# Performance work log

Measured on AMD Instinct MI355X. Metric: run time of the kernel, lower is better.

The kernel has to match this reference:

```python
import jax, jax.numpy as jnp
import numpy as np

N, D, H, C, E, M = 8192, 256, 256, 64, 262144, 2048
WD = 5e-4   # weight_decay
HP1 = 0.9
TAU = 0.5


def _l2norm(x, eps=1e-12):
    n = jnp.sqrt(jnp.sum(x * x, axis=1, keepdims=True))
    return x / jnp.maximum(n, eps)


def setup_inputs() -> dict:
    key = jax.random.key(0)
    ks = jax.random.split(key, 20)
    s = 0.05
    return dict(
        features=jax.random.uniform(ks[0], (N, D), dtype=jnp.float32),
        support=jax.random.uniform(ks[1], (N, N), dtype=jnp.float32) / N,  # mimics normalized adjacency scale
        labels=jax.random.uniform(ks[2], (N, C), dtype=jnp.float32),
        mat01_intra=jax.random.uniform(ks[3], (M, M), dtype=jnp.float32),
        mat01_inter=jax.random.uniform(ks[4], (M, M), dtype=jnp.float32),
        W0=jax.random.normal(ks[5], (D, H), dtype=jnp.float32) * s,
        b0=jnp.zeros((H,), jnp.float32),
        W1=jax.random.normal(ks[6], (H, C), dtype=jnp.float32) * s,
        b1=jnp.zeros((C,), jnp.float32),
        Wh0=jax.random.normal(ks[7], (D, H), dtype=jnp.float32) * s,
        bh0=jnp.zeros((H,), jnp.float32),
        Wh1=jax.random.normal(ks[8], (H, C), dtype=jnp.float32) * s,
        bh1=jnp.zeros((C,), jnp.float32),
        Wc=jax.random.normal(ks[9], (2 * C, 1), dtype=jnp.float32) * s,
        bc=jnp.zeros((1,), jnp.float32),
        edge_pos_i=jax.random.randint(ks[10], (E,), 0, N, dtype=jnp.int32),
        edge_pos_j=jax.random.randint(ks[11], (E,), 0, N, dtype=jnp.int32),
        train_idx=jax.random.randint(ks[12], (M,), 0, N, dtype=jnp.int32),
        mask=jax.random.randint(ks[13], (N,), 0, 2, dtype=jnp.int32),
    )


def _forward(features, support, labels, mat01_intra, mat01_inter,
             W0, b0, W1, b1, Wh0, bh0, Wh1, bh1, Wc, bc,
             edge_pos_i, edge_pos_j, train_idx, mask):
    # --- GCN branch: relu(S (X W0) + b0) -> S (h0 W1) + b1
    h0 = jax.nn.relu(support @ (features @ W0) + b0)
    h1 = support @ (h0 @ W1) + b1
    gcn_n = _l2norm(h1)
    # --- HGCN branch (2-layer GCN stand-in)
    g0 = jax.nn.relu(support @ (features @ Wh0) + bh0)
    hgcn = support @ (g0 @ Wh1) + bh1
    hgcn_n = _l2norm(hgcn)
    outputs = _l2norm(0.6 * gcn_n + 0.4 * hgcn_n)

    # masked softmax cross entropy
    maskf = mask.astype(jnp.float32)
    maskf = maskf / jnp.mean(maskf)
    logp = jax.nn.log_softmax(outputs, axis=1)
    loss_ce = jnp.mean(-jnp.sum(labels * logp, axis=1) * maskf)

    # edge gathers + contra MLP: log sigmoid of linear on concatenated pairs
    yi_g, yj_g = gcn_n[edge_pos_i], gcn_n[edge_pos_j]
    yi_h, yj_h = hgcn_n[edge_pos_i], hgcn_n[edge_pos_j]
    z1 = jnp.concatenate([yi_g, yj_h], axis=1) @ Wc + bc  # [E,1]
    z2 = jnp.concatenate([yi_h, yj_g], axis=1) @ Wc + bc
    p_e_xy = -jnp.mean(jax.nn.log_sigmoid(z1)) - jnp.mean(jax.nn.log_sigmoid(z2))

    # unsupervised contrastive over full NxN
    cd1 = jnp.exp((gcn_n @ hgcn_n.T) / TAU)      # [N,N]
    pn1 = jnp.diagonal(cd1) / jnp.mean(cd1, axis=1)
    cd2 = jnp.exp((hgcn_n @ gcn_n.T) / TAU)
    pn2 = jnp.diagonal(cd2) / jnp.mean(cd2, axis=1)
    contra = -HP1 * jnp.mean(jnp.log(jnp.concatenate([pn1, pn2], axis=0)))

    # supervised contrastive on train subset
    rowsum = jnp.sum(mat01_intra, axis=1)  # mat01_intra_rowsum buffer
    h1t, h2t = gcn_n[train_idx], hgcn_n[train_idx]
    Mn = train_idx.shape[0]

    def sup(a, b):
        hc = jnp.exp((a @ b.T) / TAU)            # [M,M]
        sp = jnp.sum(hc * mat01_intra, axis=1)
        sn = (jnp.sum(hc * mat01_inter, axis=1) + sp) / (Mn - 1)
        return (sp / rowsum) / sn

    pns = jnp.concatenate([sup(h1t, h2t), sup(h2t, h1t)], axis=0)
    contra = contra + (-HP1 * jnp.mean(jnp.log(pns)))

    wd = WD * 0.5 * (jnp.sum(W0 ** 2) + jnp.sum(b0 ** 2) + jnp.sum(W1 ** 2)
                     + jnp.sum(b1 ** 2) + jnp.sum(Wc ** 2) + jnp.sum(bc ** 2))
    loss = loss_ce + 0.4 * p_e_xy + contra + wd  # HGCN.loss = 0 for the stand-in

    correct = (jnp.argmax(outputs, axis=1) == jnp.argmax(labels, axis=1)).astype(jnp.float32)
    accuracy = jnp.mean(correct * maskf)
    return outputs, loss, accuracy


def reference(features, support, labels, mat01_intra, mat01_inter,
              W0, b0, W1, b1, Wh0, bh0, Wh1, bh1, Wc, bc,
              edge_pos_i, edge_pos_j, train_idx, mask):
    return _forward(features, support, labels, mat01_intra, mat01_inter,
                    W0, b0, W1, b1, Wh0, bh0, Wh1, bh1, Wc, bc,
                    edge_pos_i, edge_pos_j, train_idx, mask)
```

## Files before the change

### kernel.cpp

```cpp
#include <hip/hip_runtime.h>

#define DEVI __device__ __forceinline__

typedef __bf16 bf16x8 __attribute__((ext_vector_type(8)));
typedef float f32x4 __attribute__((ext_vector_type(4)));
typedef unsigned short u16;
typedef unsigned long long ull;

constexpr int NN = 8192;
constexpr int EE = 262144;

constexpr size_t OF_WT0b = 0;
constexpr size_t OF_WT1b = OF_WT0b + 65536;
constexpr size_t OF_BIA0 = OF_WT1b + 32768;
constexpr size_t OF_X16  = OF_BIA0 + 512;
constexpr size_t OF_A    = OF_X16 + 1048576;
constexpr size_t OF_B    = OF_A + 2097152;
constexpr size_t OF_C    = OF_B + 2097152;
constexpr size_t OF_D    = OF_C + 2097152;
constexpr size_t OF_VEC  = OF_D + 524288;
constexpr size_t OF_SD   = OF_VEC;
constexpr size_t OF_R1   = OF_SD + 8192;
constexpr size_t OF_R2   = OF_R1 + 16384;
constexpr size_t OF_AG   = OF_R2 + 16384;
constexpr size_t OF_BG   = OF_AG + 8192;
constexpr size_t OF_AH   = OF_BG + 8192;
constexpr size_t OF_BH   = OF_AH + 8192;
constexpr size_t OF_SP1  = OF_BH + 8192;
constexpr size_t OF_SNR1 = OF_SP1 + 2048;
constexpr size_t OF_SP2  = OF_SNR1 + 2048;
constexpr size_t OF_SNR2 = OF_SP2 + 2048;
constexpr size_t OF_RSI  = OF_SNR2 + 2048;
constexpr size_t OF_SCAL = OF_RSI + 2048;
constexpr size_t WS_SMALL = OF_SCAL + 16;
constexpr size_t OF_S16  = WS_SMALL;
constexpr size_t WS_FULL = OF_S16 + 33554432;
constexpr size_t OF_E    = WS_FULL;
constexpr size_t WS_FULL4 = OF_E + 8388608;

#define SC_CE 0
#define SC_MASK 1
#define SC_ACC 2
#define SC_E1 3
#define SC_E2 4
#define SC_C1 5
#define SC_C2 6
#define SC_WD 7

DEVI u16 bf1(float f) { __bf16 h = (__bf16)f; return __builtin_bit_cast(u16, h); }
DEVI unsigned int bf2(float a, float b) {
  return (unsigned)bf1(a) | ((unsigned)bf1(b) << 16);
}
DEVI ull bf4(float4 v) {
  return (ull)bf2(v.x, v.y) | ((ull)bf2(v.z, v.w) << 32);
}
DEVI float b2f(u16 h) { return __uint_as_float(((unsigned)h) << 16); }
DEVI float lo16(unsigned w) { return __uint_as_float(w << 16); }
DEVI float hi16(unsigned w) { return __uint_as_float(w & 0xffff0000u); }
DEVI f32x4 mfma16(bf16x8 a, bf16x8 b, f32x4 c) {
  return __builtin_amdgcn_mfma_f32_16x16x32_bf16(a, b, c, 0, 0, 0);
}
DEVI float wsum64(float v) {
  #pragma unroll
  for (int m = 1; m < 64; m <<= 1) v += __shfl_xor(v, m, 64);
  return v;
}
DEVI float wmax64(float v) {
  #pragma unroll
  for (int m = 1; m < 64; m <<= 1) v = fmaxf(v, __shfl_xor(v, m, 64));
  return v;
}
DEVI int wargmax64(float v, int idx) {
  #pragma unroll
  for (int m = 1; m < 64; m <<= 1) {
    float ov = __shfl_xor(v, m, 64);
    int   oi = __shfl_xor(idx, m, 64);
    if (ov > v || (ov == v && oi < idx)) { v = ov; idx = oi; }
  }
  return idx;
}
DEVI void blockAtomicAdd(float* dst, float v) {
  __shared__ float red[4];
  const int tid = threadIdx.x;
  v = wsum64(v);
  __syncthreads();
  if ((tid & 63) == 0) red[tid >> 6] = v;
  __syncthreads();
  if (tid == 0) atomicAdd(dst, red[0] + red[1] + red[2] + red[3]);
}
DEVI float logsig(float z) {
  return fminf(z, 0.f) - log1pf(__expf(-fabsf(z)));
}

__global__ __launch_bounds__(256)
void cvtbf(const float* __restrict__ src, u16* __restrict__ dst, long n8) {
  long stride = (long)gridDim.x * 256;
  for (long i = (long)blockIdx.x * 256 + threadIdx.x; i < n8; i += stride) {
    long off = i << 3;
    float4 a = *(const float4*)(src + off);
    float4 b = *(const float4*)(src + off + 4);
    uint4 o;
    o.x = bf2(a.x, a.y); o.y = bf2(a.z, a.w);
    o.z = bf2(b.x, b.y); o.w = bf2(b.z, b.w);
    *(uint4*)(dst + off) = o;
  }
}

__global__ void prep(const float* __restrict__ W0, const float* __restrict__ Wh0,
                     const float* __restrict__ W1, const float* __restrict__ Wh1,
                     const float* __restrict__ b0, const float* __restrict__ bh0,
                     u16* __restrict__ wt0, u16* __restrict__ wt1,
                     float* __restrict__ bias0) {
  int t = blockIdx.x * 256 + threadIdx.x;
  if (t < 131072) {
    int j = t >> 8, k = t & 255;
    wt0[t] = bf1((j < 256) ? W0[k * 256 + j] : Wh0[k * 256 + (j - 256)]);
  } else if (t < 196608) {
    int u = t - 131072;
    int j = u >> 9, k = u & 511;
    float v = 0.f;
    if (j < 64)  { if (k < 256)  v = W1 [k * 64 + j]; }
    else         { if (k >= 256) v = Wh1[(k - 256) * 64 + (j - 64)]; }
    wt1[u] = bf1(v);
  } else if (t < 197120) {
    int j = t - 196608;
    bias0[j] = (j < 256) ? b0[j] : bh0[j - 256];
  }
}

template <int FM, int FN, int SWZ, int MLOC, int NLOG>
__global__ __launch_bounds__(256, 4)
void gemm_a(const u16* __restrict__ A16, const u16* __restrict__ B16,
            u16* __restrict__ Cv, int K, int Ntot, int ksteps, size_t splitStride) {
  constexpr int BM = 32 * FM, BN = 32 * FN;
  constexpr int NSEG = (BM + BN) / 16;
  constexpr int SPW = NSEG / 4;
  __shared__ __align__(16) u16 As[2][BM * 32];
  __shared__ __align__(16) u16 Bs[2][BN * 32];
  const int tid = threadIdx.x;
  const int l = tid & 63, wid = tid >> 6;
  const int wr = wid >> 1, wc = wid & 1;
  const int fr = l & 15, fg = l >> 4;

  int m0, n0;
  if (SWZ) {
    int id = blockIdx.x + gridDim.x * blockIdx.y;
    int e = id & 7, s = id >> 3;
    m0 = (e * MLOC + (s >> NLOG)) * BM;
    n0 = (s & ((1 << NLOG) - 1)) * BN;
  } else {
    m0 = blockIdx.y * BM;
    n0 = blockIdx.x * BN;
  }
  const size_t kbase = (size_t)blockIdx.z * ksteps * 32;

  const u16* gsrc[SPW];
  u16* ld0[SPW];
  u16* ld1[SPW];
  #pragma unroll
  for (int q = 0; q < SPW; ++q) {
    int s = q * 4 + wid;
    if (s < BM / 16) {
      gsrc[q] = A16 + (size_t)(m0 + s * 16 + (l & 15)) * K + kbase + ((l >> 4) << 3);
      ld0[q] = &As[0][s << 9];
      ld1[q] = &As[1][s << 9];
    } else {
      int t2 = s - BM / 16;
      gsrc[q] = B16 + (size_t)(n0 + t2 * 16 + (l & 15)) * K + kbase + ((l >> 4) << 3);
      ld0[q] = &Bs[0][t2 << 9];
      ld1[q] = &Bs[1][t2 << 9];
    }
  }
  auto stageTo = [&](int buf, int ks2) {
    int koff = ks2 * 32;
    #pragma unroll
    for (int q = 0; q < SPW; ++q) {
      u16* d = buf ? ld1[q] : ld0[q];
      __builtin_amdgcn_global_load_lds(
          (const __attribute__((address_space(1))) void*)(gsrc[q] + koff),
          (__attribute__((address_space(3))) void*)d, 16, 0, 0);
    }
  };

  f32x4 zero = {0.f, 0.f, 0.f, 0.f};
  f32x4 acc[FM][FN];
  #pragma unroll
  for (int i = 0; i < FM; ++i)
    #pragma unroll
    for (int j = 0; j < FN; ++j) acc[i][j] = zero;

  stageTo(0, 0);
  int cur = 0;
  for (int ks = 0; ks < ksteps; ++ks) {
    __syncthreads();
    if (ks + 1 < ksteps) stageTo(cur ^ 1, ks + 1);
    bf16x8 af[FM], bfv[FN];
    #pragma unroll
    for (int i = 0; i < FM; ++i)
      af[i] = *(const bf16x8*)&As[cur][((wr * FM + i) << 9) + (l << 3)];
    #pragma unroll
    for (int j = 0; j < FN; ++j)
      bfv[j] = *(const bf16x8*)&Bs[cur][((wc * FN + j) << 9) + (l << 3)];
    #pragma unroll
    for (int i = 0; i < FM; ++i)
      #pragma unroll
      for (int j = 0; j < FN; ++j)
        acc[i][j] = mfma16(af[i], bfv[j], acc[i][j]);
    cur ^= 1;
  }

  u16* outp = Cv + (size_t)blockIdx.z * splitStride;
  #pragma unroll
  for (int i = 0; i < FM; ++i)
    #pragma unroll
    for (int j = 0; j < FN; ++j)
      #pragma unroll
      for (int r = 0; r < 4; ++r) {
        int grow = m0 + wr * 16 * FM + i * 16 + (fg << 2) + r;
        int gcol = n0 + wc * 16 * FN + j * 16 + fr;
        outp[(size_t)grow * Ntot + gcol] = bf1(acc[i][j][r]);
      }
}

template <int FM, int FN, int TA, int TB, int SWZ, int MLOC, int NLOG, int MINB>
__global__ __launch_bounds__(256, MINB)
void gemm_k(const void* __restrict__ Av, const void* __restrict__ Bv,
            u16* __restrict__ Cv, int K, int Ntot, int ksteps, size_t splitStride) {
  constexpr int BM = 32 * FM, BN = 32 * FN;
  constexpr int PAf = BM / 32, PAh = BM / 64 > 0 ? BM / 64 : 1;
  constexpr int PBf = BN / 32, PBh = BN / 64 > 0 ? BN / 64 : 1;
  __shared__ __align__(16) u16 As[2][BM * 32];
  __shared__ __align__(16) u16 Bs[2][BN * 32];
  const int tid = threadIdx.x;
  const int l = tid & 63, wid = tid >> 6;
  const int wr = wid >> 1, wc = wid & 1;
  const int fr = l & 15, fg = l >> 4;

  int m0, n0;
  if (SWZ) {
    int id = blockIdx.x + gridDim.x * blockIdx.y;
    int e = id & 7, s = id >> 3;
    m0 = (e * MLOC + (s >> NLOG)) * BM;
    n0 = (s & ((1 << NLOG) - 1)) * BN;
  } else {
    m0 = blockIdx.y * BM;
    n0 = blockIdx.x * BN;
  }
  const size_t kbase = (size_t)blockIdx.z * ksteps * 32;

  float4 ra32[TA ? 1 : PAf];
  uint4  ra16[TA ? PAh : 1];
  float4 rb32[TB ? 1 : PBf];
  uint4  rb16[TB ? PBh : 1];

  auto loadT = [&](int koff) {
    if constexpr (!TA) {
      #pragma unroll
      for (int p = 0; p < PAf; ++p) {
        int idx = p * 256 + tid;
        int lane = (idx & 127) >> 1, half = idx & 1;
        int row = ((idx >> 7) << 4) + (lane & 15);
        int kcol = ((lane >> 4) << 3) + (half << 2);
        ra32[p] = *(const float4*)((const float*)Av + (size_t)(m0 + row) * K + kbase + koff + kcol);
      }
    } else {
      #pragma unroll
      for (int p = 0; p < PAh; ++p) {
        int idx = p * 256 + tid;
        int lane = idx & 63;
        int row = ((idx >> 6) << 4) + (lane & 15);
        int kcol = (lane >> 4) << 3;
        ra16[p] = *(const uint4*)((const u16*)Av + (size_t)(m0 + row) * K + kbase + koff + kcol);
      }
    }
    if constexpr (!TB) {
      #pragma unroll
      for (int p = 0; p < PBf; ++p) {
        int idx = p * 256 + tid;
        int lane = (idx & 127) >> 1, half = idx & 1;
        int row = ((idx >> 7) << 4) + (lane & 15);
        int kcol = ((lane >> 4) << 3) + (half << 2);
        rb32[p] = *(const float4*)((const float*)Bv + (size_t)(n0 + row) * K + kbase + koff + kcol);
      }
    } else {
      #pragma unroll
      for (int p = 0; p < PBh; ++p) {
        int idx = p * 256 + tid;
        int lane = idx & 63;
        int row = ((idx >> 6) << 4) + (lane & 15);
        int kcol = (lane >> 4) << 3;
        rb16[p] = *(const uint4*)((const u16*)Bv + (size_t)(n0 + row) * K + kbase + koff + kcol);
      }
    }
  };
  auto writeT = [&](int buf) {
    if constexpr (!TA) {
      #pragma unroll
      for (int p = 0; p < PAf; ++p) {
        int idx = p * 256 + tid;
        *(ull*)&As[buf][idx << 2] = bf4(ra32[p]);
      }
    } else {
      #pragma unroll
      for (int p = 0; p < PAh; ++p) {
        int idx = p * 256 + tid;
        *(uint4*)&As[buf][idx << 3] = ra16[p];
      }
    }
    if constexpr (!TB) {
      #pragma unroll
      for (int p = 0; p < PBf; ++p) {
        int idx = p * 256 + tid;
        *(ull*)&Bs[buf][idx << 2] = bf4(rb32[p]);
      }
    } else {
      #pragma unroll
      for (int p = 0; p < PBh; ++p) {
        int idx = p * 256 + tid;
        *(uint4*)&Bs[buf][idx << 3] = rb16[p];
      }
    }
  };

  f32x4 zero = {0.f, 0.f, 0.f, 0.f};
  f32x4 acc[FM][FN];
  #pragma unroll
  for (int i = 0; i < FM; ++i)
    #pragma unroll
    for (int j = 0; j < FN; ++j) acc[i][j] = zero;

  loadT(0);
  writeT(0);
  if (ksteps > 1) loadT(32);
  __syncthreads();

  for (int ks = 0; ks < ksteps; ++ks) {
    const int cur = ks & 1;
    bf16x8 af[FM], bfv[FN];
    #pragma unroll
    for (int i = 0; i < FM; ++i)
      af[i] = *(const bf16x8*)&As[cur][((wr * FM + i) << 9) + (l << 3)];
    #pragma unroll
    for (int j = 0; j < FN; ++j)
      bfv[j] = *(const bf16x8*)&Bs[cur][((wc * FN + j) << 9) + (l << 3)];
    if (ks + 1 < ksteps) writeT(cur ^ 1);
    if (ks + 2 < ksteps) loadT((ks + 2) * 32);
    #pragma unroll
    for (int i = 0; i < FM; ++i)
      #pragma unroll
      for (int j = 0; j < FN; ++j)
        acc[i][j] = mfma16(af[i], bfv[j], acc[i][j]);
    __syncthreads();
  }

  u16* outp = Cv + (size_t)blockIdx.z * splitStride;
  #pragma unroll
  for (int i = 0; i < FM; ++i)
    #pragma unroll
    for (int j = 0; j < FN; ++j)
      #pragma unroll
      for (int r = 0; r < 4; ++r) {
        int grow = m0 + wr * 16 * FM + i * 16 + (fg << 2) + r;
        int gcol = n0 + wc * 16 * FN + j * 16 + fr;
        outp[(size_t)grow * Ntot + gcol] = bf1(acc[i][j][r]);
      }
}

template <int NS>
__global__ __launch_bounds__(256)
void relupack(const u16* __restrict__ z, const float* __restrict__ bias,
              u16* __restrict__ h16) {
  int t = blockIdx.x * 256 + threadIdx.x;
  int off = t << 3;
  int col = off & 511;
  float4 c0 = *(const float4*)(bias + col);
  float4 c1 = *(const float4*)(bias + col + 4);
  float r[8] = {c0.x, c0.y, c0.z, c0.w, c1.x, c1.y, c1.z, c1.w};
  #pragma unroll
  for (int s = 0; s < NS; ++s) {
    uint4 a = *(const uint4*)(z + (size_t)s * 8192 * 512 + off);
    r[0] += lo16(a.x); r[1] += hi16(a.x);
    r[2] += lo16(a.y); r[3] += hi16(a.y);
    r[4] += lo16(a.z); r[5] += hi16(a.z);
    r[6] += lo16(a.w); r[7] += hi16(a.w);
  }
  uint4 o;
  o.x = bf2(fmaxf(r[0], 0.f), fmaxf(r[1], 0.f));
  o.y = bf2(fmaxf(r[2], 0.f), fmaxf(r[3], 0.f));
  o.z = bf2(fmaxf(r[4], 0.f), fmaxf(r[5], 0.f));
  o.w = bf2(fmaxf(r[6], 0.f), fmaxf(r[7], 0.f));
  *(uint4*)(h16 + off) = o;
}

template <int NS>
__global__ __launch_bounds__(256)
void rowstats(const u16* __restrict__ Z2p, const float* __restrict__ b1,
              const float* __restrict__ bh1, const float* __restrict__ labels,
              const int* __restrict__ mask, const float* __restrict__ Wc,
              float* __restrict__ outp, u16* __restrict__ gcn16, u16* __restrict__ hgcn16,
              float* __restrict__ sd, float* __restrict__ ag, float* __restrict__ bg,
              float* __restrict__ ah, float* __restrict__ bh, float* __restrict__ scal) {
  const int tid = threadIdx.x, l = tid & 63, w = tid >> 6;
  const float wa = Wc[l], wb = Wc[64 + l];
  const float bb1 = b1[l], bbh1 = bh1[l];
  float s_ce = 0.f, s_mk = 0.f, s_ac = 0.f;
  for (int it = 0; it < 8; ++it) {
    int row = blockIdx.x * 32 + it * 4 + w;
    float h1 = bb1, hg = bbh1;
    #pragma unroll
    for (int s = 0; s < NS; ++s) {
      h1 += b2f(Z2p[(size_t)s * 1048576 + row * 128 + l]);
      hg += b2f(Z2p[(size_t)s * 1048576 + row * 128 + 64 + l]);
    }
    float n1 = wsum64(h1 * h1);
    float gn = h1 / fmaxf(sqrtf(n1), 1e-12f);
    float n2 = wsum64(hg * hg);
    float hn = hg / fmaxf(sqrtf(n2), 1e-12f);
    float oc = 0.6f * gn + 0.4f * hn;
    float n3 = wsum64(oc * oc);
    float o = oc / fmaxf(sqrtf(n3), 1e-12f);
    size_t ro = (size_t)row * 64 + l;
    outp[ro] = o; gcn16[ro] = bf1(gn); hgcn16[ro] = bf1(hn);
    float sdv = wsum64(gn * hn);
    float vag = wsum64(gn * wa), vbg = wsum64(gn * wb);
    float vah = wsum64(hn * wa), vbh = wsum64(hn * wb);
    float lab = labels[ro];
    float mx = wmax64(o);
    float se = wsum64(__expf(o - mx));
    float lse = mx + __logf(se);
    float slab = wsum64(lab);
    float slo = wsum64(lab * o);
    int am_o = wargmax64(o, l);
    int am_l = wargmax64(lab, l);
    if (l == 0) {
      sd[row] = sdv; ag[row] = vag; bg[row] = vbg; ah[row] = vah; bh[row] = vbh;
      float mk = (float)mask[row];
      s_ce += (lse * slab - slo) * mk;
      s_mk += mk;
      s_ac += (am_o == am_l) ? mk : 0.f;
    }
  }
  blockAtomicAdd(&scal[SC_CE], s_ce);
  blockAtomicAdd(&scal[SC_MASK], s_mk);
  blockAtomicAdd(&scal[SC_ACC], s_ac);
}

__global__ __launch_bounds__(256)
void rowsumexp2(const u16* __restrict__ G16, const u16* __restrict__ H16,
                float* __restrict__ R1, float* __restrict__ R2) {
  constexpr int PK = 72;
  __shared__ __align__(16) u16 At[64 * PK];
  __shared__ __align__(16) u16 Bt[64 * PK];
  const int bx = blockIdx.x;
  const int nh = bx >> 8, r = bx & 255, dir = r >> 7;
  const u16* __restrict__ A = dir ? H16 : G16;
  const u16* __restrict__ B = dir ? G16 : H16;
  float* __restrict__ out = (dir ? R2 : R1) + nh * 8192;
  const int tid = threadIdx.x, l = tid & 63, w = tid >> 6;
  const int m0 = (r & 127) * 64;
  #pragma unroll
  for (int p = 0; p < 2; ++p) {
    int idx = p * 256 + tid, row = idx >> 3, kq = (idx & 7) << 3;
    *(uint4*)&At[row * PK + kq] = *(const uint4*)(A + (size_t)(m0 + row) * 64 + kq);
  }
  __syncthreads();
  const int fr = l & 15, fg = l >> 4;
  bf16x8 a0 = *(const bf16x8*)&At[(w * 16 + fr) * PK + (fg << 3)];
  bf16x8 a1 = *(const bf16x8*)&At[(w * 16 + fr) * PK + 32 + (fg << 3)];
  float rs0 = 0.f, rs1 = 0.f, rs2 = 0.f, rs3 = 0.f;
  const int nbeg = nh * 4096;
  for (int n0 = nbeg; n0 < nbeg + 4096; n0 += 64) {
    __syncthreads();
    #pragma unroll
    for (int p = 0; p < 2; ++p) {
      int idx = p * 256 + tid, row = idx >> 3, kq = (idx & 7) << 3;
      *(uint4*)&Bt[row * PK + kq] = *(const uint4*)(B + (size_t)(n0 + row) * 64 + kq);
    }
    __syncthreads();
    #pragma unroll
    for (int jn = 0; jn < 4; ++jn) {
      bf16x8 b0 = *(const bf16x8*)&Bt[(jn * 16 + fr) * PK + (fg << 3)];
      bf16x8 b1 = *(const bf16x8*)&Bt[(jn * 16 + fr) * PK + 32 + (fg << 3)];
      f32x4 c = {0.f, 0.f, 0.f, 0.f};
      c = mfma16(a0, b0, c);
      c = mfma16(a1, b1, c);
      rs0 += __expf(c[0] * 2.0f);
      rs1 += __expf(c[1] * 2.0f);
      rs2 += __expf(c[2] * 2.0f);
      rs3 += __expf(c[3] * 2.0f);
    }
  }
  #pragma unroll
  for (int m = 1; m < 16; m <<= 1) {
    rs0 += __shfl_xor(rs0, m, 64);
    rs1 += __shfl_xor(rs1, m, 64);
    rs2 += __shfl_xor(rs2, m, 64);
    rs3 += __shfl_xor(rs3, m, 64);
  }
  if (fr == 0) {
    int rb = m0 + w * 16 + fg * 4;
    out[rb + 0] = rs0; out[rb + 1] = rs1; out[rb + 2] = rs2; out[rb + 3] = rs3;
  }
}

__global__ __launch_bounds__(256)
void supstats2(const u16* __restrict__ G16, const u16* __restrict__ H16,
               const int* __restrict__ tidx,
               const float* __restrict__ Wi_g, const float* __restrict__ We_g,
               float* __restrict__ SP1, float* __restrict__ SNR1,
               float* __restrict__ SP2, float* __restrict__ SNR2) {
  constexpr int PK = 72;
  __shared__ __align__(16) u16 At[64 * PK];
  __shared__ __align__(16) u16 Bt[64 * PK];
  __shared__ float Ws0[64 * 68];
  __shared__ float Ws1[64 * 68];
  const int bx = blockIdx.x;
  const int chunk = bx >> 6, sub = bx & 63, dir = sub >> 5;
  const u16* __restrict__ A = dir ? H16 : G16;
  const u16* __restrict__ B = dir ? G16 : H16;
  float* __restrict__ sp_out  = dir ? SP2 : SP1;
  float* __restrict__ sn_out  = dir ? SNR2 : SNR1;
  const int tid = threadIdx.x, l = tid & 63, w = tid >> 6;
  const int m0 = (sub & 31) * 64;
  #pragma unroll
  for (int p = 0; p < 2; ++p) {
    int idx = p * 256 + tid, row = idx >> 3, kq = (idx & 7) << 3;
    int gr = tidx[m0 + row];
    *(uint4*)&At[row * PK + kq] = *(const uint4*)(A + (size_t)gr * 64 + kq);
  }
  __syncthreads();
  const int fr = l & 15, fg = l >> 4;
  bf16x8 a0 = *(const bf16x8*)&At[(w * 16 + fr) * PK + (fg << 3)];
  bf16x8 a1 = *(const bf16x8*)&At[(w * 16 + fr) * PK + 32 + (fg << 3)];
  float sp0 = 0, sp1 = 0, sp2 = 0, sp3 = 0, sn0 = 0, sn1 = 0, sn2 = 0, sn3 = 0;
  const int nbeg = chunk * 512;
  for (int n0 = nbeg; n0 < nbeg + 512; n0 += 64) {
    __syncthreads();
    #pragma unroll
    for (int p = 0; p < 2; ++p) {
      int idx = p * 256 + tid, row = idx >> 3, kq = (idx & 7) << 3;
      int gr = tidx[n0 + row];
      *(uint4*)&Bt[row * PK + kq] = *(const uint4*)(B + (size_t)gr * 64 + kq);
    }
    #pragma unroll
    for (int p = 0; p < 4; ++p) {
      int idx = p * 256 + tid, row = idx >> 4, kq = (idx & 15) << 2;
      *(float4*)&Ws0[row * 68 + kq] = *(const float4*)(Wi_g + (size_t)(m0 + row) * 2048 + n0 + kq);
      *(float4*)&Ws1[row * 68 + kq] = *(const float4*)(We_g + (size_t)(m0 + row) * 2048 + n0 + kq);
    }
    __syncthreads();
    #pragma unroll
    for (int jn = 0; jn < 4; ++jn) {
      bf16x8 b0 = *(const bf16x8*)&Bt[(jn * 16 + fr) * PK + (fg << 3)];
      bf16x8 b1 = *(const bf16x8*)&Bt[(jn * 16 + fr) * PK + 32 + (fg << 3)];
      f32x4 c = {0.f, 0.f, 0.f, 0.f};
      c = mfma16(a0, b0, c);
      c = mfma16(a1, b1, c);
      int cl = jn * 16 + fr;
      int rl = w * 16 + fg * 4;
      float e0 = __expf(c[0] * 2.0f);
      float e1 = __expf(c[1] * 2.0f);
      float e2 = __expf(c[2] * 2.0f);
      float e3 = __expf(c[3] * 2.0f);
      sp0 += e0 * Ws0[(rl + 0) * 68 + cl]; sn0 += e0 * Ws1[(rl + 0) * 68 + cl];
      sp1 += e1 * Ws0[(rl + 1) * 68 + cl]; sn1 += e1 * Ws1[(rl + 1) * 68 + cl];
      sp2 += e2 * Ws0[(rl + 2) * 68 + cl]; sn2 += e2 * Ws1[(rl + 2) * 68 + cl];
      sp3 += e3 * Ws0[(rl + 3) * 68 + cl]; sn3 += e3 * Ws1[(rl + 3) * 68 + cl];
    }
  }
  #pragma unroll
  for (int m = 1; m < 16; m <<= 1) {
    sp0 += __shfl_xor(sp0, m, 64); sn0 += __shfl_xor(sn0, m, 64);
    sp1 += __shfl_xor(sp1, m, 64); sn1 += __shfl_xor(sn1, m, 64);
    sp2 += __shfl_xor(sp2, m, 64); sn2 += __shfl_xor(sn2, m, 64);
    sp3 += __shfl_xor(sp3, m, 64); sn3 += __shfl_xor(sn3, m, 64);
  }
  if (fr == 0) {
    int rb = m0 + w * 16 + fg * 4;
    atomicAdd(&sp_out[rb + 0], sp0); atomicAdd(&sn_out[rb + 0], sn0);
    atomicAdd(&sp_out[rb + 1], sp1); atomicAdd(&sn_out[rb + 1], sn1);
    atomicAdd(&sp_out[rb + 2], sp2); atomicAdd(&sn_out[rb + 2], sn2);
    atomicAdd(&sp_out[rb + 3], sp3); atomicAdd(&sn_out[rb + 3], sn3);
  }
}

__global__ __launch_bounds__(256)
void rowsum2048(const float* __restrict__ Wi, float* __restrict__ rsi) {
  int l = threadIdx.x & 63, w = threadIdx.x >> 6;
  int row = blockIdx.x * 4 + w;
  float s = 0.f;
  #pragma unroll
  for (int p = 0; p < 8; ++p) {
    int c = (p * 64 + l) << 2;
    float4 v = *(const float4*)(Wi + (size_t)row * 2048 + c);
    s += v.x + v.y + v.z + v.w;
  }
  s = wsum64(s);
  if (l == 0) rsi[row] = s;
}

__global__ __launch_bounds__(256)
void edgered(const int* __restrict__ ei, const int* __restrict__ ej,
             const float* __restrict__ ag, const float* __restrict__ bg,
             const float* __restrict__ ah, const float* __restrict__ bh,
             const float* __restrict__ bc, float* __restrict__ scal) {
  int t = blockIdx.x * 256 + threadIdx.x;
  float bcv = bc[0];
  float s1 = 0.f, s2 = 0.f;
  for (int e = t; e < EE; e += 65536) {
    int i = ei[e], j = ej[e];
    s1 += logsig(ag[i] + bh[j] + bcv);
    s2 += logsig(ah[i] + bg[j] + bcv);
  }
  blockAtomicAdd(&scal[SC_E1], s1);
  blockAtomicAdd(&scal[SC_E2], s2);
}

__global__ __launch_bounds__(256)
void contrared(const float* __restrict__ sd, const float* __restrict__ r1,
               const float* __restrict__ r2, float* __restrict__ scal) {
  int i = blockIdx.x * 256 + threadIdx.x;
  constexpr float LOGN = 9.01091334728f;
  float ra = r1[i] + r1[8192 + i];
  float rb = r2[i] + r2[8192 + i];
  float v = 4.f * sd[i] - __logf(ra) - __logf(rb) + 2.f * LOGN;
  blockAtomicAdd(&scal[SC_C1], v);
}

__global__ __launch_bounds__(256)
void supred(const float* __restrict__ sp1, const float* __restrict__ snr1,
            const float* __restrict__ sp2, const float* __restrict__ snr2,
            const float* __restrict__ rsi, float* __restrict__ scal) {
  int i = blockIdx.x * 256 + threadIdx.x;
  float rs = rsi[i];
  float a1 = sp1[i], d1 = (snr1[i] + a1) * (1.f / 2047.f);
  float a2 = sp2[i], d2 = (snr2[i] + a2) * (1.f / 2047.f);
  float v = __logf(a1 / rs / d1) + __logf(a2 / rs / d2);
  blockAtomicAdd(&scal[SC_C2], v);
}

__global__ __launch_bounds__(256)
void wdsum(const float* __restrict__ W0, const float* __restrict__ b0,
           const float* __restrict__ W1, const float* __restrict__ b1,
           const float* __restrict__ Wc, const float* __restrict__ bc,
           float* __restrict__ scal) {
  int t = threadIdx.x;
  float s = 0.f;
  for (int i = t; i < 16384; i += 256) {
    float4 v = *(const float4*)(W0 + i * 4);
    s += v.x * v.x + v.y * v.y + v.z * v.z + v.w * v.w;
  }
  for (int i = t; i < 4096; i += 256) {
    float4 v = *(const float4*)(W1 + i * 4);
    s += v.x * v.x + v.y * v.y + v.z * v.z + v.w * v.w;
  }
  if (t < 256) { float v = b0[t]; s += v * v; }
  if (t < 64)  { float v = b1[t]; s += v * v; }
  if (t < 128) { float v = Wc[t]; s += v * v; }
  if (t == 0)  { float v = bc[0]; s += v * v; }
  blockAtomicAdd(&scal[SC_WD], s);
}

__global__ void finalk(const float* __restrict__ scal, float* __restrict__ dst) {
  float masks = scal[SC_MASK];
  float loss = scal[SC_CE] / masks
             + 0.4f * (-(scal[SC_E1] + scal[SC_E2]) * (1.f / 262144.f))
             - 0.9f * scal[SC_C1] * (1.f / 16384.f)
             - 0.9f * scal[SC_C2] * (1.f / 4096.f)
             + 5e-4f * 0.5f * scal[SC_WD];
  dst[0] = loss;
  dst[1] = scal[SC_ACC] / masks;
}

extern "C" void kernel_launch(void* const* d_in, const int* in_sizes, int n_in,
                              void* d_out, int out_size, void* d_ws, size_t ws_size,
                              hipStream_t stream) {
  const float* features = (const float*)d_in[0];
  const float* support  = (const float*)d_in[1];
  const float* labels   = (const float*)d_in[2];
  const float* intra    = (const float*)d_in[3];
  const float* inter    = (const float*)d_in[4];
  const float* W0  = (const float*)d_in[5];
  const float* b0  = (const float*)d_in[6];
  const float* W1  = (const float*)d_in[7];
  const float* b1  = (const float*)d_in[8];
  const float* Wh0 = (const float*)d_in[9];
  const float* bh0 = (const float*)d_in[10];
  const float* Wh1 = (const float*)d_in[11];
  const float* bh1 = (const float*)d_in[12];
  const float* Wc  = (const float*)d_in[13];
  const float* bc  = (const float*)d_in[14];
  const int* ei    = (const int*)d_in[15];
  const int* ej    = (const int*)d_in[16];
  const int* tidx  = (const int*)d_in[17];
  const int* mask  = (const int*)d_in[18];

  if (ws_size < WS_SMALL * sizeof(float)) return;
  const bool big  = ws_size >= WS_FULL * sizeof(float);
  const bool big4 = ws_size >= WS_FULL4 * sizeof(float);

  float* ws = (float*)d_ws;
  u16*   WT0b  = (u16*)(ws + OF_WT0b);
  u16*   WT1b  = (u16*)(ws + OF_WT1b);
  float* BIA0  = ws + OF_BIA0;
  u16*   X16   = (u16*)(ws + OF_X16);
  u16*   XWT16 = (u16*)(ws + OF_A);
  u16*   H16   = (u16*)(ws + OF_A);
  u16*   ZbS2  = (u16*)(ws + OF_B);
  u16*   Z2p8  = (u16*)(ws + OF_B);
  u16*   HWT16 = (u16*)(ws + OF_D);
  u16*   G16   = (u16*)(ws + OF_A);
  u16*   HG16  = (u16*)(ws + OF_A + 262144);
  u16*   S16   = (u16*)(ws + OF_S16);
  u16*   ZbS4  = (u16*)(ws + OF_E);
  u16*   Z2p16 = (u16*)(ws + OF_E);
  float* SD   = ws + OF_SD;
  float* R1   = ws + OF_R1;
  float* R2   = ws + OF_R2;
  float* AG   = ws + OF_AG;
  float* BG   = ws + OF_BG;
  float* AH   = ws + OF_AH;
  float* BH   = ws + OF_BH;
  float* SP1  = ws + OF_SP1;
  float* SNR1 = ws + OF_SNR1;
  float* SP2  = ws + OF_SP2;
  float* SNR2 = ws + OF_SNR2;
  float* RSI  = ws + OF_RSI;
  float* SCAL = ws + OF_SCAL;
  float* outp = (float*)d_out;

  hipMemsetAsync(SCAL, 0, 16 * sizeof(float), stream);
  hipMemsetAsync(SP1, 0, 4 * 2048 * sizeof(float), stream);
  prep<<<770, 256, 0, stream>>>(W0, Wh0, W1, Wh1, b0, bh0, WT0b, WT1b, BIA0);
  cvtbf<<<256, 256, 0, stream>>>(features, X16, 262144);

  gemm_a<4, 4, 0, 0, 0><<<dim3(64, 4, 1), 256, 0, stream>>>(
      WT0b, X16, XWT16, 256, 8192, 8, 0);

  if (big) cvtbf<<<4096, 256, 0, stream>>>(support, S16, 8388608);

  if (big4) {
    gemm_a<4, 4, 1, 8, 2><<<dim3(4, 64, 4), 256, 0, stream>>>(
        S16, XWT16, ZbS4, 8192, 512, 64, (size_t)8192 * 512);
    relupack<4><<<2048, 256, 0, stream>>>(ZbS4, BIA0, H16);
  } else if (big) {
    gemm_a<4, 4, 1, 8, 2><<<dim3(4, 64, 2), 256, 0, stream>>>(
        S16, XWT16, ZbS2, 8192, 512, 128, (size_t)8192 * 512);
    relupack<2><<<2048, 256, 0, stream>>>(ZbS2, BIA0, H16);
  } else {
    gemm_k<4, 4, 0, 1, 1, 8, 2, 3><<<dim3(4, 64, 2), 256, 0, stream>>>(
        support, XWT16, ZbS2, 8192, 512, 128, (size_t)8192 * 512);
    relupack<2><<<2048, 256, 0, stream>>>(ZbS2, BIA0, H16);
  }

  gemm_a<2, 4, 0, 0, 0><<<dim3(64, 2, 1), 256, 0, stream>>>(
      WT1b, H16, HWT16, 512, 8192, 16, 0);

  if (big4) {
    gemm_a<4, 4, 1, 8, 0><<<dim3(1, 64, 16), 256, 0, stream>>>(
        S16, HWT16, Z2p16, 8192, 128, 16, (size_t)8192 * 128);
    rowstats<16><<<256, 256, 0, stream>>>(Z2p16, b1, bh1, labels, mask, Wc,
                                          outp, G16, HG16, SD, AG, BG, AH, BH, SCAL);
  } else if (big) {
    gemm_a<4, 4, 1, 8, 0><<<dim3(1, 64, 8), 256, 0, stream>>>(
        S16, HWT16, Z2p8, 8192, 128, 32, (size_t)8192 * 128);
    rowstats<8><<<256, 256, 0, stream>>>(Z2p8, b1, bh1, labels, mask, Wc,
                                         outp, G16, HG16, SD, AG, BG, AH, BH, SCAL);
  } else {
    gemm_k<4, 4, 0, 1, 1, 8, 0, 3><<<dim3(1, 64, 8), 256, 0, stream>>>(
        support, HWT16, Z2p8, 8192, 128, 32, (size_t)8192 * 128);
    rowstats<8><<<256, 256, 0, stream>>>(Z2p8, b1, bh1, labels, mask, Wc,
                                         outp, G16, HG16, SD, AG, BG, AH, BH, SCAL);
  }

  rowsumexp2<<<512, 256, 0, stream>>>(G16, HG16, R1, R2);
  rowsum2048<<<512, 256, 0, stream>>>(intra, RSI);
  supstats2<<<256, 256, 0, stream>>>(G16, HG16, tidx, intra, inter,
                                     SP1, SNR1, SP2, SNR2);
  edgered<<<256, 256, 0, stream>>>(ei, ej, AG, BG, AH, BH, bc, SCAL);
  contrared<<<32, 256, 0, stream>>>(SD, R1, R2, SCAL);
  supred<<<8, 256, 0, stream>>>(SP1, SNR1, SP2, SNR2, RSI, SCAL);
  wdsum<<<1, 256, 0, stream>>>(W0, b0, W1, b1, Wc, bc, SCAL);
  finalk<<<1, 1, 0, stream>>>(SCAL, outp + (size_t)8192 * 64);
}
```

Measured before the change: 457.6 us.

## Drop bf16 support copy; stream fp32 support directly with LDS-direct B loads

Removes the separate conversion of the 8192x8192 support matrix to bf16 and its cached copy. The two big support GEMMs now read fp32 support directly, convert it in registers, and stage the bf16 B operand via global_load_lds straight into shared memory. The pipeline is reordered so the sync sits at the top of each k-step. This removes one full read and write pass over support but doubles the bytes read from support in each GEMM.

```diff
diff --git a/kernel.cpp b/kernel.cpp
--- a/kernel.cpp
+++ b/kernel.cpp
@@ -15,9 +15,7 @@
 constexpr size_t OF_BIA0 = OF_WT1b + 32768;
 constexpr size_t OF_X16  = OF_BIA0 + 512;
 constexpr size_t OF_A    = OF_X16 + 1048576;
-constexpr size_t OF_B    = OF_A + 2097152;
-constexpr size_t OF_C    = OF_B + 2097152;
-constexpr size_t OF_D    = OF_C + 2097152;
+constexpr size_t OF_D    = OF_A + 2097152;
 constexpr size_t OF_VEC  = OF_D + 524288;
 constexpr size_t OF_SD   = OF_VEC;
 constexpr size_t OF_R1   = OF_SD + 8192;
@@ -33,10 +31,8 @@
 constexpr size_t OF_RSI  = OF_SNR2 + 2048;
 constexpr size_t OF_SCAL = OF_RSI + 2048;
 constexpr size_t WS_SMALL = OF_SCAL + 16;
-constexpr size_t OF_S16  = WS_SMALL;
-constexpr size_t WS_FULL = OF_S16 + 33554432;
-constexpr size_t OF_E    = WS_FULL;
-constexpr size_t WS_FULL4 = OF_E + 8388608;
+constexpr size_t OF_E    = WS_SMALL;
+constexpr size_t WS_NEED = OF_E + 8388608;
 
 #define SC_CE 0
 #define SC_MASK 1
@@ -222,13 +218,14 @@
       }
 }
 
-template <int FM, int FN, int TA, int TB, int SWZ, int MLOC, int NLOG, int MINB>
-__global__ __launch_bounds__(256, MINB)
-void gemm_k(const void* __restrict__ Av, const void* __restrict__ Bv,
+template <int FM, int FN, int SWZ, int MLOC, int NLOG>
+__global__ __launch_bounds__(256, 3)
+void gemm_f(const float* __restrict__ Af, const u16* __restrict__ B16,
             u16* __restrict__ Cv, int K, int Ntot, int ksteps, size_t splitStride) {
+  static_assert(FM == 4, "A reg-staging assumes BM=128");
   constexpr int BM = 32 * FM, BN = 32 * FN;
-  constexpr int PAf = BM / 32, PAh = BM / 64 > 0 ? BM / 64 : 1;
-  constexpr int PBf = BN / 32, PBh = BN / 64 > 0 ? BN / 64 : 1;
+  constexpr int BSEG = BN / 16;
+  constexpr int SPWB = BSEG / 4;
   __shared__ __align__(16) u16 As[2][BM * 32];
   __shared__ __align__(16) u16 Bs[2][BN * 32];
   const int tid = threadIdx.x;
@@ -248,78 +245,49 @@
   }
   const size_t kbase = (size_t)blockIdx.z * ksteps * 32;
 
-  float4 ra32[TA ? 1 : PAf];
-  uint4  ra16[TA ? PAh : 1];
-  float4 rb32[TB ? 1 : PBf];
-  uint4  rb16[TB ? PBh : 1];
-
-  auto loadT = [&](int koff) {
-    if constexpr (!TA) {
-      #pragma unroll
-      for (int p = 0; p < PAf; ++p) {
-        int idx = p * 256 + tid;
-        int lane = (idx & 127) >> 1, half = idx & 1;
-        int row = ((idx >> 7) << 4) + (lane & 15);
-        int kcol = ((lane >> 4) << 3) + (half << 2);
-        ra32[p] = *(const float4*)((const float*)Av + (size_t)(m0 + row) * K + kbase + koff + kcol);
-      }
-    } else {
-      #pragma unroll
-      for (int p = 0; p < PAh; ++p) {
-        int idx = p * 256 + tid;
-        int lane = idx & 63;
-        int row = ((idx >> 6) << 4) + (lane & 15);
-        int kcol = (lane >> 4) << 3;
-        ra16[p] = *(const uint4*)((const u16*)Av + (size_t)(m0 + row) * K + kbase + koff + kcol);
-      }
-    }
-    if constexpr (!TB) {
-      #pragma unroll
-      for (int p = 0; p < PBf; ++p) {
-        int idx = p * 256 + tid;
-        int lane = (idx & 127) >> 1, half = idx & 1;
-        int row = ((idx >> 7) << 4) + (lane & 15);
-        int kcol = ((lane >> 4) << 3) + (half << 2);
-        rb32[p] = *(const float4*)((const float*)Bv + (size_t)(n0 + row) * K + kbase + koff + kcol);
-      }
-    } else {
-      #pragma unroll
-      for (int p = 0; p < PBh; ++p) {
-        int idx = p * 256 + tid;
-        int lane = idx & 63;
-        int row = ((idx >> 6) << 4) + (lane & 15);
-        int kcol = (lane >> 4) << 3;
-        rb16[p] = *(const uint4*)((const u16*)Bv + (size_t)(n0 + row) * K + kbase + koff + kcol);
-      }
+  const int seg = tid >> 5, sub = tid & 31;
+  const float* arow = Af + (size_t)(m0 + seg * 16 + (sub & 15)) * K + kbase
+                        + ((sub >> 4) << 3);
+  const int awo0 = (seg << 9) + (sub << 3);
+  const int awo1 = (seg << 9) + ((sub + 32) << 3);
+
+  const u16* gsrcB[SPWB];
+  u16* lb0[SPWB];
+  u16* lb1[SPWB];
+  #pragma unroll
+  for (int q = 0; q < SPWB; ++q) {
+    int t2 = q * 4 + wid;
+    gsrcB[q] = B16 + (size_t)(n0 + t2 * 16 + (l & 15)) * K + kbase + ((l >> 4) << 3);
+    lb0[q] = &Bs[0][t2 << 9];
+    lb1[q] = &Bs[1][t2 << 9];
+  }
+  auto stageB = [&](int buf, int ks2) {
+    int koff = ks2 * 32;
+    #pragma unroll
+    for (int q = 0; q < SPWB; ++q) {
+      u16* d = buf ? lb1[q] : lb0[q];
+      __builtin_amdgcn_global_load_lds(
+          (const __attribute__((address_space(1))) void*)(gsrcB[q] + koff),
+          (__attribute__((address_space(3))) void*)d, 16, 0, 0);
     }
   };
-  auto writeT = [&](int buf) {
-    if constexpr (!TA) {
-      #pragma unroll
-      for (int p = 0; p < PAf; ++p) {
-        int idx = p * 256 + tid;
-        *(ull*)&As[buf][idx << 2] = bf4(ra32[p]);
-      }
-    } else {
-      #pragma unroll
-      for (int p = 0; p < PAh; ++p) {
-        int idx = p * 256 + tid;
-        *(uint4*)&As[buf][idx << 3] = ra16[p];
-      }
-    }
-    if constexpr (!TB) {
-      #pragma unroll
-      for (int p = 0; p < PBf; ++p) {
-        int idx = p * 256 + tid;
-        *(ull*)&Bs[buf][idx << 2] = bf4(rb32[p]);
-      }
-    } else {
-      #pragma unroll
-      for (int p = 0; p < PBh; ++p) {
-        int idx = p * 256 + tid;
-        *(uint4*)&Bs[buf][idx << 3] = rb16[p];
-      }
-    }
+
+  float4 ra0, ra1, ra2, ra3;
+  auto loadA = [&](int koff) {
+    const float* p = arow + koff;
+    ra0 = *(const float4*)p;
+    ra1 = *(const float4*)(p + 4);
+    ra2 = *(const float4*)(p + 16);
+    ra3 = *(const float4*)(p + 20);
+  };
+  auto writeA = [&](int buf) {
+    uint4 a, b;
+    a.x = bf2(ra0.x, ra0.y); a.y = bf2(ra0.z, ra0.w);
+    a.z = bf2(ra1.x, ra1.y); a.w = bf2(ra1.z, ra1.w);
+    b.x = bf2(ra2.x, ra2.y); b.y = bf2(ra2.z, ra2.w);
+    b.z = bf2(ra3.x, ra3.y); b.w = bf2(ra3.z, ra3.w);
+    *(uint4*)&As[buf][awo0] = a;
+    *(uint4*)&As[buf][awo1] = b;
   };
 
   f32x4 zero = {0.f, 0.f, 0.f, 0.f};
@@ -329,13 +297,19 @@
     #pragma unroll
     for (int j = 0; j < FN; ++j) acc[i][j] = zero;
 
-  loadT(0);
-  writeT(0);
-  if (ksteps > 1) loadT(32);
-  __syncthreads();
-
+  loadA(0);
+  writeA(0);
+  stageB(0, 0);
+  if (ksteps > 1) loadA(32);
+
+  int cur = 0;
   for (int ks = 0; ks < ksteps; ++ks) {
-    const int cur = ks & 1;
+    __syncthreads();
+    if (ks + 1 < ksteps) {
+      writeA(cur ^ 1);
+      stageB(cur ^ 1, ks + 1);
+    }
+    if (ks + 2 < ksteps) loadA((ks + 2) * 32);
     bf16x8 af[FM], bfv[FN];
     #pragma unroll
     for (int i = 0; i < FM; ++i)
@@ -343,14 +317,12 @@
     #pragma unroll
     for (int j = 0; j < FN; ++j)
       bfv[j] = *(const bf16x8*)&Bs[cur][((wc * FN + j) << 9) + (l << 3)];
-    if (ks + 1 < ksteps) writeT(cur ^ 1);
-    if (ks + 2 < ksteps) loadT((ks + 2) * 32);
     #pragma unroll
     for (int i = 0; i < FM; ++i)
       #pragma unroll
       for (int j = 0; j < FN; ++j)
         acc[i][j] = mfma16(af[i], bfv[j], acc[i][j]);
-    __syncthreads();
+    cur ^= 1;
   }
 
   u16* outp = Cv + (size_t)blockIdx.z * splitStride;
@@ -695,9 +667,7 @@
   const int* tidx  = (const int*)d_in[17];
   const int* mask  = (const int*)d_in[18];
 
-  if (ws_size < WS_SMALL * sizeof(float)) return;
-  const bool big  = ws_size >= WS_FULL * sizeof(float);
-  const bool big4 = ws_size >= WS_FULL4 * sizeof(float);
+  if (ws_size < WS_NEED * sizeof(float)) return;
 
   float* ws = (float*)d_ws;
   u16*   WT0b  = (u16*)(ws + OF_WT0b);
@@ -706,12 +676,9 @@
   u16*   X16   = (u16*)(ws + OF_X16);
   u16*   XWT16 = (u16*)(ws + OF_A);
   u16*   H16   = (u16*)(ws + OF_A);
-  u16*   ZbS2  = (u16*)(ws + OF_B);
-  u16*   Z2p8  = (u16*)(ws + OF_B);
   u16*   HWT16 = (u16*)(ws + OF_D);
   u16*   G16   = (u16*)(ws + OF_A);
   u16*   HG16  = (u16*)(ws + OF_A + 262144);
-  u16*   S16   = (u16*)(ws + OF_S16);
   u16*   ZbS4  = (u16*)(ws + OF_E);
   u16*   Z2p16 = (u16*)(ws + OF_E);
   float* SD   = ws + OF_SD;
@@ -737,41 +704,17 @@
   gemm_a<4, 4, 0, 0, 0><<<dim3(64, 4, 1), 256, 0, stream>>>(
       WT0b, X16, XWT16, 256, 8192, 8, 0);
 
-  if (big) cvtbf<<<4096, 256, 0, stream>>>(support, S16, 8388608);
-
-  if (big4) {
-    gemm_a<4, 4, 1, 8, 2><<<dim3(4, 64, 4), 256, 0, stream>>>(
-        S16, XWT16, ZbS4, 8192, 512, 64, (size_t)8192 * 512);
-    relupack<4><<<2048, 256, 0, stream>>>(ZbS4, BIA0, H16);
-  } else if (big) {
-    gemm_a<4, 4, 1, 8, 2><<<dim3(4, 64, 2), 256, 0, stream>>>(
-        S16, XWT16, ZbS2, 8192, 512, 128, (size_t)8192 * 512);
-    relupack<2><<<2048, 256, 0, stream>>>(ZbS2, BIA0, H16);
-  } else {
-    gemm_k<4, 4, 0, 1, 1, 8, 2, 3><<<dim3(4, 64, 2), 256, 0, stream>>>(
-        support, XWT16, ZbS2, 8192, 512, 128, (size_t)8192 * 512);
-    relupack<2><<<2048, 256, 0, stream>>>(ZbS2, BIA0, H16);
-  }
+  gemm_f<4, 4, 1, 8, 2><<<dim3(4, 64, 4), 256, 0, stream>>>(
+      support, XWT16, ZbS4, 8192, 512, 64, (size_t)8192 * 512);
+  relupack<4><<<2048, 256, 0, stream>>>(ZbS4, BIA0, H16);
 
   gemm_a<2, 4, 0, 0, 0><<<dim3(64, 2, 1), 256, 0, stream>>>(
       WT1b, H16, HWT16, 512, 8192, 16, 0);
 
-  if (big4) {
-    gemm_a<4, 4, 1, 8, 0><<<dim3(1, 64, 16), 256, 0, stream>>>(
-        S16, HWT16, Z2p16, 8192, 128, 16, (size_t)8192 * 128);
-    rowstats<16><<<256, 256, 0, stream>>>(Z2p16, b1, bh1, labels, mask, Wc,
-                                          outp, G16, HG16, SD, AG, BG, AH, BH, SCAL);
-  } else if (big) {
-    gemm_a<4, 4, 1, 8, 0><<<dim3(1, 64, 8), 256, 0, stream>>>(
-        S16, HWT16, Z2p8, 8192, 128, 32, (size_t)8192 * 128);
-    rowstats<8><<<256, 256, 0, stream>>>(Z2p8, b1, bh1, labels, mask, Wc,
-                                         outp, G16, HG16, SD, AG, BG, AH, BH, SCAL);
-  } else {
-    gemm_k<4, 4, 0, 1, 1, 8, 0, 3><<<dim3(1, 64, 8), 256, 0, stream>>>(
-        support, HWT16, Z2p8, 8192, 128, 32, (size_t)8192 * 128);
-    rowstats<8><<<256, 256, 0, stream>>>(Z2p8, b1, bh1, labels, mask, Wc,
-                                         outp, G16, HG16, SD, AG, BG, AH, BH, SCAL);
-  }
+  gemm_f<4, 4, 1, 8, 0><<<dim3(1, 64, 16), 256, 0, stream>>>(
+      support, HWT16, Z2p16, 8192, 128, 16, (size_t)8192 * 128);
+  rowstats<16><<<256, 256, 0, stream>>>(Z2p16, b1, bh1, labels, mask, Wc,
+                                        outp, G16, HG16, SD, AG, BG, AH, BH, SCAL);
 
   rowsumexp2<<<512, 256, 0, stream>>>(G16, HG16, R1, R2);
   rowsum2048<<<512, 256, 0, stream>>>(intra, RSI);
```

Result: slower. 495.3 us (+8.2%).
